# Kernel tuning notes

Hardware: AMD Instinct MI355X
Metric: run time of the kernel (lower is better)

The kernel has to match this reference:

```python
import jax, jax.numpy as jnp
import numpy as np

RADIUS = 0.4
SIGMA = 0.08
DIM_OUT = 64


def setup_inputs() -> dict:
    key = jax.random.key(0)
    k1, k2, k3, k4 = jax.random.split(key, 4)
    m, b, nc, ks, na = 1024, 2, 64, 13, 20
    frag = jax.random.uniform(k1, (m, 3), dtype=jnp.float32)          # (m,3) raw points in unit cube
    clouds = jax.random.uniform(k2, (b, 3, nc), dtype=jnp.float32)    # (b,3,nc) == n_center -> no FPS
    # anchor-rotated kernel points, |p| <= 0.7*radius (KERNEL_CONDENSE_RATIO)
    kernels = (jax.random.uniform(k3, (ks, na, 3), dtype=jnp.float32) - 0.5) * (2.0 * 0.7 * RADIUS)
    # BasicSO3Conv weight, xavier_normal with relu gain on (dim_out, 1, ks): std = sqrt(2)*sqrt(2/(ks + dim_out*ks))
    std = np.sqrt(2.0) * np.sqrt(2.0 / (ks + DIM_OUT * ks))
    W = jax.random.normal(k4, (DIM_OUT, ks), dtype=jnp.float32) * std
    return {"frag": frag, "clouds": clouds, "kernels": kernels, "W": W}


def reference(frag, clouds, kernels, W):
    # frag (m,3), clouds (b,3,nc), kernels (ks,na,3), W (dim_out, ks)
    centers = clouds                                   # clouds.shape[2] == n_center -> skip FPS
    c = jnp.transpose(centers, (0, 2, 1))              # (b,nc,3)
    b, nc, _ = c.shape
    ks, na, _ = kernels.shape

    # ball query: points within radius of each center
    d2c = jnp.sum((frag[None, :, None, :] - c[:, None, :, :]) ** 2, axis=-1)   # (b,m,nc)
    mask = (d2c < RADIUS * RADIUS).astype(frag.dtype)                          # (b,m,nc)
    nnctn = jnp.sum(mask, axis=1)                                              # (b,nc)

    # gaussian weight of each in-ball point w.r.t. each rotated kernel point location
    kpos = c[:, :, None, None, :] + kernels[None, None, :, :, :]               # (b,nc,ks,na,3)
    fn2 = jnp.sum(frag * frag, axis=-1)                                        # (m,)
    pn2 = jnp.sum(kpos * kpos, axis=-1)                                        # (b,nc,ks,na)
    dot = jnp.einsum('md,bnkad->bmnka', frag, kpos)                            # (b,m,nc,ks,na)
    d2k = fn2[None, :, None, None, None] + pn2[:, None] - 2.0 * dot            # (b,m,nc,ks,na)
    w = jnp.exp(-d2k / (2.0 * SIGMA)) * mask[:, :, :, None, None]

    wts = jnp.transpose(jnp.sum(w, axis=1), (0, 2, 1, 3))                      # (b,ks,nc,na)
    wts = wts / (nnctn[:, None, :, None] + 1.0)

    # BasicSO3Conv: view (b, dim_in*ks, nc*na), W @ x, view back (dim_in=1)
    x = wts.reshape(b, ks, nc * na)
    feats = jnp.einsum('ok,bkp->bop', W, x).reshape(b, W.shape[0], nc, na)     # (b,dim_out,nc,na)
    return feats
```

## Files before the change

### kernel.cpp

```cpp
#include <hip/hip_runtime.h>
#include <hip/hip_bf16.h>

#define M_PTS   1024
#define B_SZ    2
#define NC      64
#define KS      13
#define NA      20
#define KA      (KS * NA)
#define DIM_OUT 64

static constexpr float R2       = 0.4f * 0.4f;
static constexpr float INV2SIG  = 6.25f;

__global__ __launch_bounds__(256)
void KernelPropagation_24206435681031_kernel(const float* __restrict__ frag,
                                             const float* __restrict__ clouds,
                                             const float* __restrict__ kernels,
                                             const float* __restrict__ W,
                                             float* __restrict__ out)
{
    const int bc = blockIdx.x;
    const int b  = bc / NC;
    const int n  = bc % NC;
    const int tid = threadIdx.x;

    const float cx = clouds[(b * 3 + 0) * NC + n];
    const float cy = clouds[(b * 3 + 1) * NC + n];
    const float cz = clouds[(b * 3 + 2) * NC + n];

    __shared__ float px[M_PTS], py[M_PTS], pz[M_PTS];
    __shared__ float kpx[KA], kpy[KA], kpz[KA];
    __shared__ float acc[KA];
    __shared__ int   cnt;

    if (tid == 0) cnt = 0;

    for (int i = tid; i < KA; i += 256) {
        kpx[i] = cx + kernels[i * 3 + 0];
        kpy[i] = cy + kernels[i * 3 + 1];
        kpz[i] = cz + kernels[i * 3 + 2];
    }
    __syncthreads();

    for (int i = tid; i < M_PTS; i += 256) {
        const float x = frag[i * 3 + 0];
        const float y = frag[i * 3 + 1];
        const float z = frag[i * 3 + 2];
        const float dx = x - cx, dy = y - cy, dz = z - cz;
        const float d2 = dx * dx + dy * dy + dz * dz;
        if (d2 < R2) {
            const int idx = atomicAdd(&cnt, 1);
            px[idx] = x; py[idx] = y; pz[idx] = z;
        }
    }
    __syncthreads();

    const int   npts = cnt;
    const float inv  = 1.0f / ((float)npts + 1.0f);

    for (int i = tid; i < KA; i += 256) {
        const float kx = kpx[i], ky = kpy[i], kz = kpz[i];
        float s = 0.0f;
        for (int j = 0; j < npts; ++j) {
            const float dx = px[j] - kx;
            const float dy = py[j] - ky;
            const float dz = pz[j] - kz;
            const float d2 = dx * dx + dy * dy + dz * dz;
            s += __expf(-d2 * INV2SIG);
        }
        acc[i] = s * inv;
    }
    __syncthreads();

    for (int i = tid; i < DIM_OUT * NA; i += 256) {
        const int o = i / NA;
        const int a = i % NA;
        float f = 0.0f;
#pragma unroll
        for (int k = 0; k < KS; ++k)
            f += W[o * KS + k] * acc[k * NA + a];
        out[((b * DIM_OUT + o) * NC + n) * NA + a] = f;
    }
}

extern "C" void kernel_launch(void* const* d_in, const int* in_sizes, int n_in,
                              void* d_out, int out_size, void* d_ws, size_t ws_size,
                              hipStream_t stream) {
    const float* frag    = (const float*)d_in[0];
    const float* clouds  = (const float*)d_in[1];
    const float* kernels = (const float*)d_in[2];
    const float* W       = (const float*)d_in[3];
    float* out = (float*)d_out;

    (void)in_sizes; (void)n_in; (void)out_size; (void)d_ws; (void)ws_size;

    KernelPropagation_24206435681031_kernel<<<B_SZ * NC, 256, 0, stream>>>(
        frag, clouds, kernels, W, out);
}
```

Before: 79.00 us.

## Expand Gaussian distance algebraically, use wave-ballot compaction and one thread per kernel point

Rewrites the Gaussian as exp2 of a dot product plus precomputed per-point and per-kernel-point terms. The per-pair work becomes three FMAs and one exp2, with the kernel-point factor kept in registers. Ball-query compaction now uses wave ballot and popcount with one atomic per wave. Points are packed as float4 in shared memory, W is staged in LDS, and the block grows to 320 threads so all 260 kernel points run in one pass. The expanded form changes floating-point rounding slightly, and 60 of the 320 threads sit idle in the main loop.

```diff
diff --git a/kernel.cpp b/kernel.cpp
--- a/kernel.cpp
+++ b/kernel.cpp
@@ -8,77 +8,111 @@
 #define NA      20
 #define KA      (KS * NA)
 #define DIM_OUT 64
+#define NTHREADS 320
 
-static constexpr float R2       = 0.4f * 0.4f;
-static constexpr float INV2SIG  = 6.25f;
+static constexpr float R2    = 0.4f * 0.4f;
+static constexpr float C2SIG = 6.25f * 1.44269504088896340736f;
 
-__global__ __launch_bounds__(256)
+__global__ __launch_bounds__(NTHREADS)
 void KernelPropagation_24206435681031_kernel(const float* __restrict__ frag,
                                              const float* __restrict__ clouds,
                                              const float* __restrict__ kernels,
                                              const float* __restrict__ W,
                                              float* __restrict__ out)
 {
-    const int bc = blockIdx.x;
-    const int b  = bc / NC;
-    const int n  = bc % NC;
-    const int tid = threadIdx.x;
+    const int bc   = blockIdx.x;
+    const int b    = bc / NC;
+    const int n    = bc % NC;
+    const int tid  = threadIdx.x;
+    const int lane = tid & 63;
+
+    __shared__ float4 pf[M_PTS];
+    __shared__ float  acc[KA];
+    __shared__ float  Wl[DIM_OUT * KS];
+    __shared__ int    cnt;
 
     const float cx = clouds[(b * 3 + 0) * NC + n];
     const float cy = clouds[(b * 3 + 1) * NC + n];
     const float cz = clouds[(b * 3 + 2) * NC + n];
 
-    __shared__ float px[M_PTS], py[M_PTS], pz[M_PTS];
-    __shared__ float kpx[KA], kpy[KA], kpz[KA];
-    __shared__ float acc[KA];
-    __shared__ int   cnt;
+    float kx2 = 0.f, ky2 = 0.f, kz2 = 0.f, ek = 0.f;
+    if (tid < KA) {
+        const float kx = cx + kernels[tid * 3 + 0];
+        const float ky = cy + kernels[tid * 3 + 1];
+        const float kz = cz + kernels[tid * 3 + 2];
+        const float pn2 = kx * kx + ky * ky + kz * kz;
+        ek  = exp2f(-C2SIG * pn2);
+        kx2 = (2.0f * C2SIG) * kx;
+        ky2 = (2.0f * C2SIG) * ky;
+        kz2 = (2.0f * C2SIG) * kz;
+    }
+
+    for (int i = tid; i < DIM_OUT * KS; i += NTHREADS) Wl[i] = W[i];
 
     if (tid == 0) cnt = 0;
-
-    for (int i = tid; i < KA; i += 256) {
-        kpx[i] = cx + kernels[i * 3 + 0];
-        kpy[i] = cy + kernels[i * 3 + 1];
-        kpz[i] = cz + kernels[i * 3 + 2];
-    }
     __syncthreads();
 
-    for (int i = tid; i < M_PTS; i += 256) {
-        const float x = frag[i * 3 + 0];
-        const float y = frag[i * 3 + 1];
-        const float z = frag[i * 3 + 2];
-        const float dx = x - cx, dy = y - cy, dz = z - cz;
-        const float d2 = dx * dx + dy * dy + dz * dz;
-        if (d2 < R2) {
-            const int idx = atomicAdd(&cnt, 1);
-            px[idx] = x; py[idx] = y; pz[idx] = z;
+    for (int base = 0; base < M_PTS; base += NTHREADS) {
+        const int i = base + tid;
+        bool  in = false;
+        float x = 0.f, y = 0.f, z = 0.f, af = 0.f;
+        if (i < M_PTS) {
+            x = frag[i * 3 + 0];
+            y = frag[i * 3 + 1];
+            z = frag[i * 3 + 2];
+            const float dx = x - cx, dy = y - cy, dz = z - cz;
+            in = (dx * dx + dy * dy + dz * dz) < R2;
+            af = -C2SIG * (x * x + y * y + z * z);
         }
+        const unsigned long long mask = __ballot(in);
+        const int tot = __popcll(mask);
+        const int pre = __popcll(mask & ((1ull << lane) - 1ull));
+        int wbase = 0;
+        if (lane == 0 && tot) wbase = atomicAdd(&cnt, tot);
+        wbase = __shfl(wbase, 0, 64);
+        if (in) pf[wbase + pre] = make_float4(x, y, z, af);
     }
     __syncthreads();
 
     const int   npts = cnt;
     const float inv  = 1.0f / ((float)npts + 1.0f);
 
-    for (int i = tid; i < KA; i += 256) {
-        const float kx = kpx[i], ky = kpy[i], kz = kpz[i];
+    if (tid < KA) {
         float s = 0.0f;
-        for (int j = 0; j < npts; ++j) {
-            const float dx = px[j] - kx;
-            const float dy = py[j] - ky;
-            const float dz = pz[j] - kz;
-            const float d2 = dx * dx + dy * dy + dz * dz;
-            s += __expf(-d2 * INV2SIG);
+        int j = 0;
+        for (; j + 1 < npts; j += 2) {
+            const float4 p0 = pf[j];
+            const float4 p1 = pf[j + 1];
+            float t0 = p0.x * kx2;
+            t0 = fmaf(p0.y, ky2, t0);
+            t0 = fmaf(p0.z, kz2, t0);
+            t0 += p0.w;
+            float t1 = p1.x * kx2;
+            t1 = fmaf(p1.y, ky2, t1);
+            t1 = fmaf(p1.z, kz2, t1);
+            t1 += p1.w;
+            s = fmaf(ek, exp2f(t0), s);
+            s = fmaf(ek, exp2f(t1), s);
         }
-        acc[i] = s * inv;
+        if (j < npts) {
+            const float4 p0 = pf[j];
+            float t0 = p0.x * kx2;
+            t0 = fmaf(p0.y, ky2, t0);
+            t0 = fmaf(p0.z, kz2, t0);
+            t0 += p0.w;
+            s = fmaf(ek, exp2f(t0), s);
+        }
+        acc[tid] = s * inv;
     }
     __syncthreads();
 
-    for (int i = tid; i < DIM_OUT * NA; i += 256) {
+    for (int i = tid; i < DIM_OUT * NA; i += NTHREADS) {
         const int o = i / NA;
         const int a = i % NA;
         float f = 0.0f;
 #pragma unroll
         for (int k = 0; k < KS; ++k)
-            f += W[o * KS + k] * acc[k * NA + a];
+            f = fmaf(Wl[o * KS + k], acc[k * NA + a], f);
         out[((b * DIM_OUT + o) * NC + n) * NA + a] = f;
     }
 }
@@ -94,6 +128,6 @@
 
     (void)in_sizes; (void)n_in; (void)out_size; (void)d_ws; (void)ws_size;
 
-    KernelPropagation_24206435681031_kernel<<<B_SZ * NC, 256, 0, stream>>>(
+    KernelPropagation_24206435681031_kernel<<<B_SZ * NC, NTHREADS, 0, stream>>>(
         frag, clouds, kernels, W, out);
 }
```

Result: faster. 72.98 us (-7.6%).

## Split each center across blocks, expand Gaussian as exp2 dot-product, ballot compaction

Applied to the files above, without the earlier changes.

Launches five single-wavefront blocks per center, each owning four anchors across all kernel points, so there are many more blocks in flight. The old version kept the last threads of its only block busy with one leftover item. The squared distance is rewritten as a dot product plus precomputed point and kernel norms, folded into exp2, and points are stored as float4 in shared memory. Shared-memory atomic compaction is replaced by wavefront ballot/popcount compaction, and results are written with float4 stores. The cost is that every block repeats the 1024-point ball query, and 12 of the 64 lanes sit idle in the exp loop.

```diff
diff --git a/kernel.cpp b/kernel.cpp
--- a/kernel.cpp
+++ b/kernel.cpp
@@ -6,81 +6,105 @@
 #define NC      64
 #define KS      13
 #define NA      20
-#define KA      (KS * NA)
 #define DIM_OUT 64
 
-static constexpr float R2       = 0.4f * 0.4f;
-static constexpr float INV2SIG  = 6.25f;
+#define NBLK_PER_C 5
+#define A_SLICE    4
+#define NITEMS     (KS * A_SLICE)
 
-__global__ __launch_bounds__(256)
+static constexpr float R2    = 0.4f * 0.4f;
+static constexpr float C2SIG = 6.25f * 1.44269504088896340736f;
+
+__global__ __launch_bounds__(64)
 void KernelPropagation_24206435681031_kernel(const float* __restrict__ frag,
                                              const float* __restrict__ clouds,
                                              const float* __restrict__ kernels,
                                              const float* __restrict__ W,
                                              float* __restrict__ out)
 {
-    const int bc = blockIdx.x;
+    const int g  = blockIdx.x;
+    const int bc = g / NBLK_PER_C;
+    const int sl = g % NBLK_PER_C;
     const int b  = bc / NC;
     const int n  = bc % NC;
-    const int tid = threadIdx.x;
+    const int t  = threadIdx.x;
+
+    __shared__ float4 pf[M_PTS];
+    __shared__ float  accs[NITEMS];
 
     const float cx = clouds[(b * 3 + 0) * NC + n];
     const float cy = clouds[(b * 3 + 1) * NC + n];
     const float cz = clouds[(b * 3 + 2) * NC + n];
 
-    __shared__ float px[M_PTS], py[M_PTS], pz[M_PTS];
-    __shared__ float kpx[KA], kpy[KA], kpz[KA];
-    __shared__ float acc[KA];
-    __shared__ int   cnt;
+    float kx2 = 0.f, ky2 = 0.f, kz2 = 0.f, ek = 0.f;
+    if (t < NITEMS) {
+        const int k = t >> 2;
+        const int a = sl * A_SLICE + (t & 3);
+        const int ki = (k * NA + a) * 3;
+        const float kx = cx + kernels[ki + 0];
+        const float ky = cy + kernels[ki + 1];
+        const float kz = cz + kernels[ki + 2];
+        const float pn2 = kx * kx + ky * ky + kz * kz;
+        ek  = exp2f(-C2SIG * pn2);
+        kx2 = (2.0f * C2SIG) * kx;
+        ky2 = (2.0f * C2SIG) * ky;
+        kz2 = (2.0f * C2SIG) * kz;
+    }
 
-    if (tid == 0) cnt = 0;
-
-    for (int i = tid; i < KA; i += 256) {
-        kpx[i] = cx + kernels[i * 3 + 0];
-        kpy[i] = cy + kernels[i * 3 + 1];
-        kpz[i] = cz + kernels[i * 3 + 2];
-    }
-    __syncthreads();
-
-    for (int i = tid; i < M_PTS; i += 256) {
+    int wbase = 0;
+    for (int base = 0; base < M_PTS; base += 64) {
+        const int i = base + t;
         const float x = frag[i * 3 + 0];
         const float y = frag[i * 3 + 1];
         const float z = frag[i * 3 + 2];
         const float dx = x - cx, dy = y - cy, dz = z - cz;
-        const float d2 = dx * dx + dy * dy + dz * dz;
-        if (d2 < R2) {
-            const int idx = atomicAdd(&cnt, 1);
-            px[idx] = x; py[idx] = y; pz[idx] = z;
-        }
+        const bool in = (dx * dx + dy * dy + dz * dz) < R2;
+        const unsigned long long mask = __ballot(in);
+        const int pre = __popcll(mask & ((1ull << t) - 1ull));
+        if (in)
+            pf[wbase + pre] = make_float4(x, y, z, -C2SIG * (x * x + y * y + z * z));
+        wbase += __popcll(mask);
     }
     __syncthreads();
 
-    const int   npts = cnt;
+    const int   npts = wbase;
     const float inv  = 1.0f / ((float)npts + 1.0f);
 
-    for (int i = tid; i < KA; i += 256) {
-        const float kx = kpx[i], ky = kpy[i], kz = kpz[i];
-        float s = 0.0f;
-        for (int j = 0; j < npts; ++j) {
-            const float dx = px[j] - kx;
-            const float dy = py[j] - ky;
-            const float dz = pz[j] - kz;
-            const float d2 = dx * dx + dy * dy + dz * dz;
-            s += __expf(-d2 * INV2SIG);
-        }
-        acc[i] = s * inv;
+    float s0 = 0.f, s1 = 0.f;
+    int j = 0;
+    for (; j + 3 < npts; j += 4) {
+        const float4 p0 = pf[j + 0];
+        const float4 p1 = pf[j + 1];
+        const float4 p2 = pf[j + 2];
+        const float4 p3 = pf[j + 3];
+        float t0 = fmaf(p0.z, kz2, fmaf(p0.y, ky2, p0.x * kx2)) + p0.w;
+        float t1 = fmaf(p1.z, kz2, fmaf(p1.y, ky2, p1.x * kx2)) + p1.w;
+        float t2 = fmaf(p2.z, kz2, fmaf(p2.y, ky2, p2.x * kx2)) + p2.w;
+        float t3 = fmaf(p3.z, kz2, fmaf(p3.y, ky2, p3.x * kx2)) + p3.w;
+        s0 = fmaf(ek, exp2f(t0), s0);
+        s1 = fmaf(ek, exp2f(t1), s1);
+        s0 = fmaf(ek, exp2f(t2), s0);
+        s1 = fmaf(ek, exp2f(t3), s1);
     }
+    for (; j < npts; ++j) {
+        const float4 p0 = pf[j];
+        float t0 = fmaf(p0.z, kz2, fmaf(p0.y, ky2, p0.x * kx2)) + p0.w;
+        s0 = fmaf(ek, exp2f(t0), s0);
+    }
+    if (t < NITEMS) accs[t] = (s0 + s1) * inv;
     __syncthreads();
 
-    for (int i = tid; i < DIM_OUT * NA; i += 256) {
-        const int o = i / NA;
-        const int a = i % NA;
-        float f = 0.0f;
+    float f0 = 0.f, f1 = 0.f, f2 = 0.f, f3 = 0.f;
 #pragma unroll
-        for (int k = 0; k < KS; ++k)
-            f += W[o * KS + k] * acc[k * NA + a];
-        out[((b * DIM_OUT + o) * NC + n) * NA + a] = f;
+    for (int k = 0; k < KS; ++k) {
+        const float w = W[t * KS + k];
+        f0 = fmaf(w, accs[k * 4 + 0], f0);
+        f1 = fmaf(w, accs[k * 4 + 1], f1);
+        f2 = fmaf(w, accs[k * 4 + 2], f2);
+        f3 = fmaf(w, accs[k * 4 + 3], f3);
     }
+    float4* dst = (float4*)(out + ((size_t)(b * DIM_OUT + t) * NC + n) * NA + sl * A_SLICE);
+    *dst = make_float4(f0, f1, f2, f3);
 }
 
 extern "C" void kernel_launch(void* const* d_in, const int* in_sizes, int n_in,
@@ -94,6 +118,6 @@
 
     (void)in_sizes; (void)n_in; (void)out_size; (void)d_ws; (void)ws_size;
 
-    KernelPropagation_24206435681031_kernel<<<B_SZ * NC, 256, 0, stream>>>(
+    KernelPropagation_24206435681031_kernel<<<B_SZ * NC * NBLK_PER_C, 64, 0, stream>>>(
         frag, clouds, kernels, W, out);
 }
```

Result: faster. 74.71 us (-5.4%).
